# Kernel optimization log

Hardware: AMD Instinct MI355X
Metric: run time of the kernel (lower is better)

Reference implementation:

```python
import jax, jax.numpy as jnp
import numpy as np

T, H = 2048, 1024          # tokens, hidden_size
NH, NKV, D = 16, 4, 64     # heads, kv heads, head_dim
E, F = 8, 1024             # experts, intermediate_size
TOPK = 1
EPS = 1e-5
THETA = 500000.0
SCALE = D ** -0.5


def rmsnorm(x, w=None, eps=EPS):
    # fp32 accumulation like vLLM RMSNorm
    v = jnp.mean(x.astype(jnp.float32) ** 2, axis=-1, keepdims=True)
    y = x.astype(jnp.float32) * jax.lax.rsqrt(v + eps)
    y = y.astype(x.dtype)
    return y * w if w is not None else y


def setup_inputs() -> dict:
    key = jax.random.key(0)
    ks = jax.random.split(key, 12)
    s = 1.0 / np.sqrt(H)
    sf = 1.0 / np.sqrt(F)
    return {
        "positions": jnp.arange(T, dtype=jnp.int32),
        "hidden_states": jax.random.normal(ks[0], (T, H), jnp.float32),
        "ln1_w": jnp.ones((H,), jnp.float32),
        "ln2_w": jnp.ones((H,), jnp.float32),
        "wqkv": jax.random.normal(ks[1], (H, (NH + 2 * NKV) * D), jnp.float32) * s,
        "wo": jax.random.normal(ks[2], (NH * D, H), jnp.float32) * s,
        "router_w": jax.random.normal(ks[3], (H, E), jnp.float32) * s,
        "w_gate": jax.random.normal(ks[4], (E, H, F), jnp.float32) * s,
        "w_up": jax.random.normal(ks[5], (E, H, F), jnp.float32) * s,
        "w_down": jax.random.normal(ks[6], (E, F, H), jnp.float32) * sf,
        "sh_gate": jax.random.normal(ks[7], (H, F), jnp.float32) * s,
        "sh_up": jax.random.normal(ks[8], (H, F), jnp.float32) * s,
        "sh_down": jax.random.normal(ks[9], (F, H), jnp.float32) * sf,
    }


def reference(positions, hidden_states, ln1_w, ln2_w, wqkv, wo, router_w,
              w_gate, w_up, w_down, sh_gate, sh_up, sh_down):
    # --- input_layernorm (residual is None on first call) ---
    residual = hidden_states
    h = rmsnorm(hidden_states, ln1_w)

    # --- attention: qkv proj ---
    qkv = h @ wqkv
    q = qkv[:, : NH * D].reshape(T, NH, D)
    k = qkv[:, NH * D: (NH + NKV) * D].reshape(T, NKV, D)
    v = qkv[:, (NH + NKV) * D:].reshape(T, NKV, D)

    # --- neox-style RoPE ---
    half = D // 2
    inv_freq = 1.0 / (THETA ** (jnp.arange(half, dtype=jnp.float32) / half))
    ang = positions.astype(jnp.float32)[:, None] * inv_freq[None, :]
    cos = jnp.cos(ang)[:, None, :]  # [T,1,half]
    sin = jnp.sin(ang)[:, None, :]

    def rope(x):
        x1, x2 = x[..., :half], x[..., half:]
        return jnp.concatenate([x1 * cos - x2 * sin, x2 * cos + x1 * sin], axis=-1)

    q = rope(q)
    k = rope(k)

    # --- fp32 QK-RMSNorm (no weight), applied after RoPE as in source ---
    q = rmsnorm(q)
    k = rmsnorm(k)

    # --- GQA causal attention ---
    n_rep = NH // NKV
    kr = jnp.repeat(k, n_rep, axis=1)  # [T,NH,D]
    vr = jnp.repeat(v, n_rep, axis=1)
    scores = jnp.einsum('thd,shd->hts', q, kr) * SCALE  # [NH,T,T]
    causal = positions[:, None] >= positions[None, :]
    scores = jnp.where(causal[None], scores, -jnp.inf)
    attn = jax.nn.softmax(scores, axis=-1)
    ao = jnp.einsum('hts,shd->thd', attn, vr).reshape(T, NH * D)
    h = ao @ wo

    # --- post_attention_layernorm with fused residual add ---
    x = h + residual
    residual = x
    h = rmsnorm(x, ln2_w)

    # --- MoE: top-1 sigmoid router, router weight applied on input ---
    logits = h @ router_w                      # [T,E]
    score, idx = jax.lax.top_k(logits, TOPK)   # [T,1]
    gate = jax.nn.sigmoid(score.astype(jnp.float32)).astype(h.dtype)
    x_in = h * gate                            # apply_router_weight_on_input
    onehot = (idx == jnp.arange(E)[None, :]).astype(h.dtype)  # [T,E]
    g = jax.nn.silu(jnp.einsum('th,ehf->tef', x_in, w_gate)) \
        * jnp.einsum('th,ehf->tef', x_in, w_up)               # [T,E,F]
    out_e = jnp.einsum('tef,efh->teh', g, w_down)             # [T,E,H]
    routed = jnp.einsum('teh,te->th', out_e, onehot)

    # --- shared expert (SiLU MLP) ---
    shared = (jax.nn.silu(h @ sh_gate) * (h @ sh_up)) @ sh_down

    out = routed + shared
    return (out, residual)
```

## Files before the change

kernel.cpp:

```cpp
#include <hip/hip_runtime.h>
#include <hip/hip_bf16.h>
#include <cmath>
#include <cstdint>

#define T 2048
#define H 1024
#define NH 16
#define NKV 4
#define DH 64
#define NE 8
#define FF 1024
#define QKVN ((NH + 2 * NKV) * DH)
#define EPS 1e-5f
#define ATTN_SCALE 0.125f
#define LOG2E 1.44269504f
#define MBOUND 12.0f
#define ASPLIT 4

typedef short bf16x8 __attribute__((ext_vector_type(8)));
typedef float floatx4 __attribute__((ext_vector_type(4)));

__device__ __forceinline__ void gload16(const void* g, void* l) {
  __builtin_amdgcn_global_load_lds((const __attribute__((address_space(1))) void*)g,
                                   (__attribute__((address_space(3))) void*)l, 16, 0, 0);
}

__global__ __launch_bounds__(256) void rmsnorm1024(const float* __restrict__ x,
                                                   const float* __restrict__ w,
                                                   __hip_bfloat16* __restrict__ yb) {
  int row = blockIdx.x;
  const float4* x4 = (const float4*)(x + (size_t)row * H);
  float4 v = x4[threadIdx.x];
  float s = v.x * v.x + v.y * v.y + v.z * v.z + v.w * v.w;
  #pragma unroll
  for (int o = 32; o; o >>= 1) s += __shfl_down(s, o, 64);
  __shared__ float red[4];
  if ((threadIdx.x & 63) == 0) red[threadIdx.x >> 6] = s;
  __syncthreads();
  s = red[0] + red[1] + red[2] + red[3];
  float inv = rsqrtf(s * (1.0f / (float)H) + EPS);
  float4 wv = ((const float4*)w)[threadIdx.x];
  __hip_bfloat16* yp = yb + (size_t)row * H + threadIdx.x * 4;
  yp[0] = __float2bfloat16(v.x * inv * wv.x);
  yp[1] = __float2bfloat16(v.y * inv * wv.y);
  yp[2] = __float2bfloat16(v.z * inv * wv.z);
  yp[3] = __float2bfloat16(v.w * inv * wv.w);
}

__global__ __launch_bounds__(256) void rms_h2(const float* __restrict__ x,
                                              const float* __restrict__ w,
                                              float* __restrict__ yf,
                                              __hip_bfloat16* __restrict__ yb,
                                              int* __restrict__ counts_g) {
  int row = blockIdx.x;
  if (row == 0 && threadIdx.x < 2 * NE) counts_g[threadIdx.x] = 0;
  float4 v = ((const float4*)(x + (size_t)row * H))[threadIdx.x];
  float s = v.x * v.x + v.y * v.y + v.z * v.z + v.w * v.w;
  #pragma unroll
  for (int o = 32; o; o >>= 1) s += __shfl_down(s, o, 64);
  __shared__ float red[4];
  if ((threadIdx.x & 63) == 0) red[threadIdx.x >> 6] = s;
  __syncthreads();
  s = red[0] + red[1] + red[2] + red[3];
  float inv = rsqrtf(s * (1.0f / (float)H) + EPS);
  float4 wv = ((const float4*)w)[threadIdx.x];
  float o0 = v.x * inv * wv.x, o1 = v.y * inv * wv.y, o2 = v.z * inv * wv.z, o3 = v.w * inv * wv.w;
  ((float4*)(yf + (size_t)row * H))[threadIdx.x] = make_float4(o0, o1, o2, o3);
  __hip_bfloat16* yp = yb + (size_t)row * H + threadIdx.x * 4;
  yp[0] = __float2bfloat16(o0);
  yp[1] = __float2bfloat16(o1);
  yp[2] = __float2bfloat16(o2);
  yp[3] = __float2bfloat16(o3);
}

__global__ __launch_bounds__(256) void tcast9(const float* __restrict__ srcE,
                                              const float* __restrict__ srcS,
                                              __hip_bfloat16* __restrict__ dst, int R, int C,
                                              long long srcStride, long long dstStride,
                                              long long sBatch, long long dBatch) {
  int z = blockIdx.z;
  const float* src = (srcS && z == (int)gridDim.z - 1) ? srcS : srcE + (long long)z * sBatch;
  dst += (long long)z * dBatch;
  int c0 = blockIdx.x * 64, r0 = blockIdx.y * 32;
  __shared__ float tile[32][65];
  int tid = threadIdx.x;
  int lr = tid >> 4;
  int lc = (tid & 15) * 4;
  #pragma unroll
  for (int it = 0; it < 2; it++) {
    float4 v = *(const float4*)(src + (long long)(r0 + lr + it * 16) * srcStride + c0 + lc);
    tile[lr + it * 16][lc + 0] = v.x;
    tile[lr + it * 16][lc + 1] = v.y;
    tile[lr + it * 16][lc + 2] = v.z;
    tile[lr + it * 16][lc + 3] = v.w;
  }
  __syncthreads();
  int oc = tid >> 2;
  int rr = (tid & 3) * 8;
  short ov[8];
  #pragma unroll
  for (int i = 0; i < 8; i++) {
    __hip_bfloat16 b = __float2bfloat16(tile[rr + i][oc]);
    ov[i] = *(short*)&b;
  }
  *(bf16x8*)((short*)dst + (long long)(c0 + oc) * dstStride + r0 + rr) = *(bf16x8*)ov;
}

__global__ __launch_bounds__(256) void gemm_bf16(const __hip_bfloat16* __restrict__ A,
                                                 const __hip_bfloat16* __restrict__ A2,
                                                 const __hip_bfloat16* __restrict__ Bt,
                                                 void* __restrict__ Cout, void* __restrict__ Cout2,
                                                 int M, int N, int K, int out_bf16,
                                                 const int* __restrict__ row_offs,
                                                 long long strideB,
                                                 const int* __restrict__ permA,
                                                 const float* __restrict__ gatev,
                                                 const float* __restrict__ addC) {
  int e = blockIdx.z;
  bool sh = (A2 != nullptr && e == (int)gridDim.z - 1);
  int rbeg = 0, rend = M;
  const __hip_bfloat16* Ap = A;
  void* Cp = Cout;
  const int* pA = permA;
  if (sh) {
    Ap = A2; Cp = Cout2; pA = nullptr;
  } else if (row_offs) {
    rbeg = row_offs[e]; rend = row_offs[e + 1];
  }
  long long m0 = rbeg + (long long)blockIdx.y * 128;
  if (m0 >= rend) return;
  long long n0 = (long long)blockIdx.x * 64;
  const __hip_bfloat16* Bp = Bt + (long long)e * strideB;

  __shared__ unsigned short As[2][128 * 64];
  __shared__ unsigned short Bs[2][64 * 64];

  int tid = threadIdx.x;
  int lane = tid & 63, w = tid >> 6;
  int wr = (w >> 1) * 64, wc = (w & 1) * 32;
  int qd = lane >> 4, ln16 = lane & 15;
  int l7 = ln16 & 7;

  floatx4 acc[4][2];
  floatx4 zero = {0.f, 0.f, 0.f, 0.f};
  #pragma unroll
  for (int i = 0; i < 4; i++)
    #pragma unroll
    for (int j = 0; j < 2; j++) acc[i][j] = zero;

  int rowA[4], kcA[4];
  const unsigned short* Arow[4];
  const unsigned short* Brow[2];
  #pragma unroll
  for (int it = 0; it < 4; it++) {
    int chunk = tid + it * 256;
    rowA[it] = chunk >> 3;
    kcA[it] = ((chunk & 7) ^ (rowA[it] & 7)) * 8;
    long long ra = m0 + rowA[it];
    if (ra >= rend) ra = rend - 1;
    long long tok = pA ? (long long)pA[ra] : ra;
    Arow[it] = (const unsigned short*)Ap + tok * K;
  }
  #pragma unroll
  for (int it = 0; it < 2; it++)
    Brow[it] = (const unsigned short*)Bp + (n0 + rowA[it]) * K;

  #pragma unroll
  for (int it = 0; it < 4; it++)
    gload16(Arow[it] + kcA[it], As[0] + (tid + it * 256) * 8);
  #pragma unroll
  for (int it = 0; it < 2; it++)
    gload16(Brow[it] + kcA[it], Bs[0] + (tid + it * 256) * 8);
  __syncthreads();

  int cur = 0;
  for (int k0 = 0; k0 < K; k0 += 64) {
    int kn = k0 + 64;
    if (kn < K) {
      #pragma unroll
      for (int it = 0; it < 4; it++)
        gload16(Arow[it] + kn + kcA[it], As[cur ^ 1] + (tid + it * 256) * 8);
      #pragma unroll
      for (int it = 0; it < 2; it++)
        gload16(Brow[it] + kn + kcA[it], Bs[cur ^ 1] + (tid + it * 256) * 8);
    }
    const unsigned short* Ac = As[cur];
    const unsigned short* Bc = Bs[cur];
    #pragma unroll
    for (int s = 0; s < 2; s++) {
      bf16x8 af[4], bfr[2];
      #pragma unroll
      for (int i = 0; i < 4; i++) {
        int row = wr + i * 16 + ln16;
        af[i] = *(const bf16x8*)(Ac + row * 64 + (((s * 4 + qd) ^ l7) * 8));
      }
      #pragma unroll
      for (int j = 0; j < 2; j++) {
        int row = wc + j * 16 + ln16;
        bfr[j] = *(const bf16x8*)(Bc + row * 64 + (((s * 4 + qd) ^ l7) * 8));
      }
      #pragma unroll
      for (int i = 0; i < 4; i++)
        #pragma unroll
        for (int j = 0; j < 2; j++)
          acc[i][j] = __builtin_amdgcn_mfma_f32_16x16x32_bf16(af[i], bfr[j], acc[i][j], 0, 0, 0);
    }
    __syncthreads();
    cur ^= 1;
  }

  #pragma unroll
  for (int i = 0; i < 4; i++) {
    #pragma unroll
    for (int r = 0; r < 4; r++) {
      long long gm = m0 + wr + i * 16 + qd * 4 + r;
      if (gm < rend) {
        float gsc = 1.0f;
        if (pA && gatev) gsc = gatev[pA[gm]];
        #pragma unroll
        for (int j = 0; j < 2; j++) {
          long long gn = n0 + wc + j * 16 + ln16;
          float v = acc[i][j][r] * gsc;
          if (addC) v += addC[gm * N + gn];
          if (out_bf16)
            ((__hip_bfloat16*)Cp)[gm * N + gn] = __float2bfloat16(v);
          else
            ((float*)Cp)[gm * N + gn] = v;
        }
      }
    }
  }
}

__global__ __launch_bounds__(256) void gemm_qkv(const __hip_bfloat16* __restrict__ A,
                                                const __hip_bfloat16* __restrict__ Bt,
                                                const int* __restrict__ positions,
                                                __hip_bfloat16* __restrict__ Qb,
                                                __hip_bfloat16* __restrict__ Kb,
                                                __hip_bfloat16* __restrict__ VtG) {
  const int K = H;
  long long m0 = (long long)blockIdx.y * 128;
  long long n0 = (long long)blockIdx.x * 64;

  __shared__ unsigned short As[2][128 * 64];
  __shared__ unsigned short Bs[2][64 * 64];

  int tid = threadIdx.x;
  int lane = tid & 63, w = tid >> 6;
  int qd = lane >> 4, ln16 = lane & 15;
  int l7 = ln16 & 7;

  floatx4 acc[2][4];
  floatx4 zero = {0.f, 0.f, 0.f, 0.f};
  #pragma unroll
  for (int i = 0; i < 2; i++)
    #pragma unroll
    for (int j = 0; j < 4; j++) acc[i][j] = zero;

  int rowA[4], kcA[4];
  const unsigned short* Arow[4];
  const unsigned short* Brow[2];
  #pragma unroll
  for (int it = 0; it < 4; it++) {
    int chunk = tid + it * 256;
    rowA[it] = chunk >> 3;
    kcA[it] = ((chunk & 7) ^ (rowA[it] & 7)) * 8;
    Arow[it] = (const unsigned short*)A + (m0 + rowA[it]) * K;
  }
  #pragma unroll
  for (int it = 0; it < 2; it++)
    Brow[it] = (const unsigned short*)Bt + (n0 + rowA[it]) * K;

  #pragma unroll
  for (int it = 0; it < 4; it++)
    gload16(Arow[it] + kcA[it], As[0] + (tid + it * 256) * 8);
  #pragma unroll
  for (int it = 0; it < 2; it++)
    gload16(Brow[it] + kcA[it], Bs[0] + (tid + it * 256) * 8);
  __syncthreads();

  int cur = 0;
  for (int k0 = 0; k0 < K; k0 += 64) {
    int kn = k0 + 64;
    if (kn < K) {
      #pragma unroll
      for (int it = 0; it < 4; it++)
        gload16(Arow[it] + kn + kcA[it], As[cur ^ 1] + (tid + it * 256) * 8);
      #pragma unroll
      for (int it = 0; it < 2; it++)
        gload16(Brow[it] + kn + kcA[it], Bs[cur ^ 1] + (tid + it * 256) * 8);
    }
    const unsigned short* Ac = As[cur];
    const unsigned short* Bc = Bs[cur];
    #pragma unroll
    for (int s = 0; s < 2; s++) {
      bf16x8 af[2], bfr[4];
      #pragma unroll
      for (int i = 0; i < 2; i++) {
        int row = w * 32 + i * 16 + ln16;
        af[i] = *(const bf16x8*)(Ac + row * 64 + (((s * 4 + qd) ^ l7) * 8));
      }
      #pragma unroll
      for (int j = 0; j < 4; j++) {
        int row = j * 16 + ln16;
        bfr[j] = *(const bf16x8*)(Bc + row * 64 + (((s * 4 + qd) ^ l7) * 8));
      }
      #pragma unroll
      for (int i = 0; i < 2; i++)
        #pragma unroll
        for (int j = 0; j < 4; j++)
          acc[i][j] = __builtin_amdgcn_mfma_f32_16x16x32_bf16(af[i], bfr[j], acc[i][j], 0, 0, 0);
    }
    __syncthreads();
    cur ^= 1;
  }

  int hh = blockIdx.x;
  if (hh < NH + NKV) {
    bool isq = hh < NH;
    float invf0 = exp2f(-(float)ln16 * (18.93156857f / 32.0f));
    float invf1 = exp2f(-(float)(ln16 + 16) * (18.93156857f / 32.0f));
    #pragma unroll
    for (int i = 0; i < 2; i++) {
      #pragma unroll
      for (int r = 0; r < 4; r++) {
        int t = (int)m0 + w * 32 + i * 16 + qd * 4 + r;
        float pos = (float)positions[t];
        float c0, s0, c1, s1;
        __sincosf(pos * invf0, &s0, &c0);
        __sincosf(pos * invf1, &s1, &c1);
        float v0 = acc[i][0][r], v1 = acc[i][1][r], v2 = acc[i][2][r], v3 = acc[i][3][r];
        float ro0 = v0 * c0 - v2 * s0;
        float ro1 = v1 * c1 - v3 * s1;
        float ro2 = v2 * c0 + v0 * s0;
        float ro3 = v3 * c1 + v1 * s1;
        float sq = ro0 * ro0 + ro1 * ro1 + ro2 * ro2 + ro3 * ro3;
        sq += __shfl_xor(sq, 1, 64);
        sq += __shfl_xor(sq, 2, 64);
        sq += __shfl_xor(sq, 4, 64);
        sq += __shfl_xor(sq, 8, 64);
        float inv = rsqrtf(sq * (1.0f / (float)DH) + EPS);
        if (isq) inv *= (ATTN_SCALE * LOG2E);
        __hip_bfloat16* dst = isq ? (Qb + (size_t)t * (NH * DH) + hh * DH)
                                  : (Kb + (size_t)t * (NKV * DH) + (hh - NH) * DH);
        dst[0 * 16 + ln16] = __float2bfloat16(ro0 * inv);
        dst[1 * 16 + ln16] = __float2bfloat16(ro1 * inv);
        dst[2 * 16 + ln16] = __float2bfloat16(ro2 * inv);
        dst[3 * 16 + ln16] = __float2bfloat16(ro3 * inv);
      }
    }
  } else {
    unsigned short* sw = ((unsigned short*)As) + w * 2560;
    #pragma unroll
    for (int i = 0; i < 2; i++)
      #pragma unroll
      for (int j = 0; j < 4; j++)
        #pragma unroll
        for (int r = 0; r < 4; r++) {
          __hip_bfloat16 b = __float2bfloat16(acc[i][j][r]);
          sw[(j * 16 + ln16) * 40 + i * 16 + qd * 4 + r] = *(unsigned short*)&b;
        }
    int d = lane;
    int t0 = (int)m0 + w * 32;
    const unsigned short* sr = sw + d * 40;
    unsigned short* vd = (unsigned short*)VtG + (size_t)((hh - NH - NKV) * DH + d) * T + t0;
    #pragma unroll
    for (int kk = 0; kk < 4; kk++) {
      short tmp[8];
      #pragma unroll
      for (int q2 = 0; q2 < 8; q2++) tmp[q2] = sr[kk * 8 + q2];
      *(bf16x8*)(vd + kk * 8) = *(bf16x8*)tmp;
    }
  }
}

__global__ __launch_bounds__(256, 2) void attn_mfma(const __hip_bfloat16* __restrict__ Qb,
                                                    const __hip_bfloat16* __restrict__ Kbuf,
                                                    const __hip_bfloat16* __restrict__ VtG,
                                                    float* __restrict__ Opart,
                                                    float* __restrict__ Lpart) {
  int kvh = blockIdx.y;
  int qi = blockIdx.x;
  int sp = blockIdx.z;
  int q0 = qi * 64;
  int nt = qi + 1;
  if (sp >= nt) return;

  __shared__ unsigned short Ks[2][64 * 64];
  __shared__ unsigned short Vs[2][64 * 64];
  __shared__ unsigned short Ps[4 * 16 * 64];

  int tid = threadIdx.x;
  int lane = tid & 63, w = tid >> 6;
  int h = kvh * 4 + w;
  int qd = lane >> 4, ln16 = lane & 15;
  int l7 = ln16 & 7;
  unsigned short* Pw = Ps + w * 16 * 64;

  int r0 = tid >> 3;
  int sc = ((tid & 7) ^ (r0 & 7)) * 8;

  const unsigned short* KbP = (const unsigned short*)Kbuf;
  const unsigned short* VtP = (const unsigned short*)VtG;

  bf16x8 aq[4][2];
  #pragma unroll
  for (int rt = 0; rt < 4; rt++) {
    const unsigned short* qp =
        (const unsigned short*)Qb + (size_t)(q0 + rt * 16 + ln16) * (NH * DH) + h * DH;
    aq[rt][0] = *(const bf16x8*)(qp + qd * 8);
    aq[rt][1] = *(const bf16x8*)(qp + 32 + qd * 8);
  }

  bf16x8 ones;
  #pragma unroll
  for (int i = 0; i < 8; i++) ones[i] = (short)0x3F80;

  floatx4 O_[4][4], accl[4];
  floatx4 zero = {0.f, 0.f, 0.f, 0.f};
  #pragma unroll
  for (int rt = 0; rt < 4; rt++) {
    #pragma unroll
    for (int j = 0; j < 4; j++) O_[rt][j] = zero;
    accl[rt] = zero;
  }

  {
    int kb = sp * 64;
    gload16(KbP + (size_t)(kb + r0) * (NKV * DH) + kvh * DH + sc, Ks[0] + tid * 8);
    gload16(KbP + (size_t)(kb + r0 + 32) * (NKV * DH) + kvh * DH + sc, Ks[0] + tid * 8 + 2048);
    gload16(VtP + (size_t)(kvh * DH + r0) * T + kb + sc, Vs[0] + tid * 8);
    gload16(VtP + (size_t)(kvh * DH + r0 + 32) * T + kb + sc, Vs[0] + tid * 8 + 2048);
  }
  __syncthreads();

  int cur = 0;
  for (int kt = sp; kt < nt; kt += ASPLIT) {
    int ktn = kt + ASPLIT;
    if (ktn < nt) {
      int kb = ktn * 64;
      unsigned short* Kn = Ks[cur ^ 1];
      unsigned short* Vn = Vs[cur ^ 1];
      gload16(KbP + (size_t)(kb + r0) * (NKV * DH) + kvh * DH + sc, Kn + tid * 8);
      gload16(KbP + (size_t)(kb + r0 + 32) * (NKV * DH) + kvh * DH + sc, Kn + tid * 8 + 2048);
      gload16(VtP + (size_t)(kvh * DH + r0) * T + kb + sc, Vn + tid * 8);
      gload16(VtP + (size_t)(kvh * DH + r0 + 32) * T + kb + sc, Vn + tid * 8 + 2048);
    }
    const unsigned short* Kc = Ks[cur];
    const unsigned short* Vc = Vs[cur];
    int kb = kt * 64;

    #pragma unroll
    for (int rt = 0; rt < 4; rt++) {
      floatx4 S_[4];
      #pragma unroll
      for (int j = 0; j < 4; j++) S_[j] = zero;
      #pragma unroll
      for (int s = 0; s < 2; s++) {
        bf16x8 bk[4];
        #pragma unroll
        for (int j = 0; j < 4; j++)
          bk[j] = *(const bf16x8*)(Kc + (j * 16 + ln16) * 64 + (((s * 4 + qd) ^ l7) * 8));
        #pragma unroll
        for (int j = 0; j < 4; j++)
          S_[j] = __builtin_amdgcn_mfma_f32_16x16x32_bf16(aq[rt][s], bk[j], S_[j], 0, 0, 0);
      }

      int tq_base = q0 + rt * 16 + qd * 4;
      if (kb + 63 > q0 + rt * 16) {
        #pragma unroll
        for (int j = 0; j < 4; j++) {
          int tk = kb + j * 16 + ln16;
          #pragma unroll
          for (int r = 0; r < 4; r++)
            S_[j][r] = (tk <= tq_base + r) ? exp2f(S_[j][r] - MBOUND) : 0.f;
        }
      } else {
        #pragma unroll
        for (int j = 0; j < 4; j++)
          #pragma unroll
          for (int r = 0; r < 4; r++) S_[j][r] = exp2f(S_[j][r] - MBOUND);
      }

      #pragma unroll
      for (int j = 0; j < 4; j++)
        #pragma unroll
        for (int r = 0; r < 4; r++) {
          int row = qd * 4 + r;
          int pc = (((j * 2 + (ln16 >> 3)) ^ (row & 7)) * 8) + l7;
          __hip_bfloat16 pb = __float2bfloat16(S_[j][r]);
          Pw[row * 64 + pc] = *(unsigned short*)&pb;
        }

      #pragma unroll
      for (int s = 0; s < 2; s++) {
        bf16x8 ap = *(const bf16x8*)(Pw + ln16 * 64 + (((s * 4 + qd) ^ l7) * 8));
        bf16x8 bv[4];
        #pragma unroll
        for (int j = 0; j < 4; j++)
          bv[j] = *(const bf16x8*)(Vc + (j * 16 + ln16) * 64 + (((s * 4 + qd) ^ l7) * 8));
        #pragma unroll
        for (int j = 0; j < 4; j++)
          O_[rt][j] = __builtin_amdgcn_mfma_f32_16x16x32_bf16(ap, bv[j], O_[rt][j], 0, 0, 0);
        accl[rt] = __builtin_amdgcn_mfma_f32_16x16x32_bf16(ap, ones, accl[rt], 0, 0, 0);
      }
    }
    __syncthreads();
    cur ^= 1;
  }

  size_t pbase = ((size_t)(qi * NH + h) * ASPLIT + sp) * (64 * 64);
  #pragma unroll
  for (int rt = 0; rt < 4; rt++) {
    int rl_base = rt * 16 + qd * 4;
    #pragma unroll
    for (int j = 0; j < 4; j++)
      #pragma unroll
      for (int r = 0; r < 4; r++)
        Opart[pbase + (size_t)(rl_base + r) * 64 + j * 16 + ln16] = O_[rt][j][r];
  }
  if (ln16 == 0) {
    size_t lbase = ((size_t)(qi * NH + h) * ASPLIT + sp) * 64;
    #pragma unroll
    for (int rt = 0; rt < 4; rt++)
      #pragma unroll
      for (int r = 0; r < 4; r++) Lpart[lbase + rt * 16 + qd * 4 + r] = accl[rt][r];
  }
}

__global__ __launch_bounds__(256) void attn_combine(const float* __restrict__ Opart,
                                                    const float* __restrict__ Lpart,
                                                    __hip_bfloat16* __restrict__ ao) {
  int qi = blockIdx.x, h = blockIdx.y;
  int nv = (qi + 1 < ASPLIT) ? (qi + 1) : ASPLIT;
  int row = threadIdx.x >> 2;
  int c0 = (threadIdx.x & 3) * 16;
  size_t base = (size_t)(qi * NH + h) * ASPLIT * 4096;
  size_t lb = (size_t)(qi * NH + h) * ASPLIT * 64;
  float l = 0.f;
  float acc[16];
  #pragma unroll
  for (int i = 0; i < 16; i++) acc[i] = 0.f;
  for (int s = 0; s < nv; s++) {
    const float* Op = Opart + base + (size_t)s * 4096 + (size_t)row * 64 + c0;
    l += Lpart[lb + s * 64 + row];
    #pragma unroll
    for (int i = 0; i < 16; i += 4) {
      float4 v = *(const float4*)(Op + i);
      acc[i] += v.x; acc[i + 1] += v.y; acc[i + 2] += v.z; acc[i + 3] += v.w;
    }
  }
  float inv = 1.f / l;
  int t = qi * 64 + row;
  short ov[16];
  #pragma unroll
  for (int i = 0; i < 16; i++) {
    __hip_bfloat16 b = __float2bfloat16(acc[i] * inv);
    ov[i] = *(short*)&b;
  }
  short* dst = (short*)ao + (size_t)t * (NH * DH) + h * DH + c0;
  *(bf16x8*)dst = *(bf16x8*)&ov[0];
  *(bf16x8*)(dst + 8) = *(bf16x8*)&ov[8];
}

__global__ __launch_bounds__(256) void silumul_both(const __hip_bfloat16* __restrict__ gA2,
                                                    const __hip_bfloat16* __restrict__ gS2,
                                                    __hip_bfloat16* __restrict__ gP,
                                                    __hip_bfloat16* __restrict__ gPs,
                                                    int n8each) {
  int i = blockIdx.x * blockDim.x + threadIdx.x;
  const __hip_bfloat16* src = gA2;
  __hip_bfloat16* dst = gP;
  if (i >= n8each) {
    i -= n8each;
    src = gS2;
    dst = gPs;
  }
  int el = i * 8;
  int row = el >> 10;
  int c = el & (FF - 1);
  const unsigned short* g = (const unsigned short*)src + (size_t)row * (2 * FF) + c;
  bf16x8 a8 = *(const bf16x8*)g;
  bf16x8 b8 = *(const bf16x8*)(g + FF);
  short o8[8];
  #pragma unroll
  for (int k = 0; k < 8; k++) {
    short sa = a8[k], sb = b8[k];
    float av = __bfloat162float(*(__hip_bfloat16*)&sa);
    float bv = __bfloat162float(*(__hip_bfloat16*)&sb);
    __hip_bfloat16 ob = __float2bfloat16(av / (1.f + __expf(-av)) * bv);
    o8[k] = *(short*)&ob;
  }
  *(bf16x8*)((unsigned short*)dst + el) = *(bf16x8*)o8;
}

__global__ __launch_bounds__(64) void router_kernel(const float* __restrict__ h2,
                                                    const float* __restrict__ rw,
                                                    int* __restrict__ idx,
                                                    float* __restrict__ gate,
                                                    int* __restrict__ counts) {
  int t = blockIdx.x;
  int lane = threadIdx.x;
  float acc[NE] = {};
  for (int k = lane; k < H; k += 64) {
    float hv = h2[(long long)t * H + k];
    float4 r0 = *(const float4*)(rw + (long long)k * NE);
    float4 r1 = *(const float4*)(rw + (long long)k * NE + 4);
    acc[0] += hv * r0.x; acc[1] += hv * r0.y; acc[2] += hv * r0.z; acc[3] += hv * r0.w;
    acc[4] += hv * r1.x; acc[5] += hv * r1.y; acc[6] += hv * r1.z; acc[7] += hv * r1.w;
  }
  #pragma unroll
  for (int off = 32; off; off >>= 1)
    #pragma unroll
    for (int e2 = 0; e2 < NE; e2++) acc[e2] += __shfl_down(acc[e2], off, 64);
  if (lane == 0) {
    int best = 0;
    float bv = acc[0];
    #pragma unroll
    for (int e2 = 1; e2 < NE; e2++)
      if (acc[e2] > bv) { bv = acc[e2]; best = e2; }
    idx[t] = best;
    gate[t] = 1.f / (1.f + expf(-bv));
    atomicAdd(&counts[best], 1);
  }
}

__global__ __launch_bounds__(256) void assign_scan(const int* __restrict__ counts,
                                                   const int* __restrict__ idx,
                                                   int* __restrict__ offs,
                                                   int* __restrict__ cnt2,
                                                   int* __restrict__ perm,
                                                   int* __restrict__ pos) {
  __shared__ int offs_s[NE + 1];
  if (threadIdx.x == 0) {
    int s = 0;
    for (int e2 = 0; e2 < NE; e2++) { offs_s[e2] = s; offs[e2] = s; s += counts[e2]; }
    offs_s[NE] = s; offs[NE] = s;
  }
  __syncthreads();
  for (int t = threadIdx.x; t < T; t += 256) {
    int e2 = idx[t];
    int p = offs_s[e2] + atomicAdd(&cnt2[e2], 1);
    pos[t] = p;
    perm[p] = t;
  }
}

__global__ __launch_bounds__(256) void final_add_kernel(float* __restrict__ out,
                                                        const float* __restrict__ outp,
                                                        const int* __restrict__ pos) {
  int t = blockIdx.x;
  int p = pos[t];
  const float4* src = (const float4*)(outp + (long long)p * H);
  float4* dst = (float4*)(out + (long long)t * H);
  float4 a = dst[threadIdx.x];
  float4 b = src[threadIdx.x];
  a.x += b.x; a.y += b.y; a.z += b.z; a.w += b.w;
  dst[threadIdx.x] = a;
}

extern "C" void kernel_launch(void* const* d_in, const int* in_sizes, int n_in,
                              void* d_out, int out_size, void* d_ws, size_t ws_size,
                              hipStream_t stream) {
  const int* positions = (const int*)d_in[0];
  const float* hidden = (const float*)d_in[1];
  const float* ln1_w = (const float*)d_in[2];
  const float* ln2_w = (const float*)d_in[3];
  const float* wqkv = (const float*)d_in[4];
  const float* wo = (const float*)d_in[5];
  const float* router_w = (const float*)d_in[6];
  const float* w_gate = (const float*)d_in[7];
  const float* w_up = (const float*)d_in[8];
  const float* w_down = (const float*)d_in[9];
  const float* sh_gate = (const float*)d_in[10];
  const float* sh_up = (const float*)d_in[11];
  const float* sh_down = (const float*)d_in[12];

  float* out = (float*)d_out;
  float* resid = out + (size_t)T * H;

  char* p = (char*)d_ws;
  auto alloc = [&](size_t bytes) { char* r = p; p += (bytes + 255) & ~(size_t)255; return r; };

  float* qkv = (float*)alloc((size_t)T * QKVN * 4);
  float* h2 = (float*)alloc((size_t)T * H * 4);
  float* gb1 = (float*)alloc((size_t)T * H * 4);
  float* outp = (float*)alloc((size_t)T * H * 4);
  __hip_bfloat16* h1b = (__hip_bfloat16*)alloc((size_t)T * H * 2);
  __hip_bfloat16* aob = (__hip_bfloat16*)alloc((size_t)T * H * 2);
  __hip_bfloat16* h2b = (__hip_bfloat16*)alloc((size_t)T * H * 2);
  __hip_bfloat16* gA2 = (__hip_bfloat16*)alloc((size_t)T * 2 * FF * 2);
  __hip_bfloat16* gP = (__hip_bfloat16*)alloc((size_t)T * FF * 2);
  __hip_bfloat16* Qb = (__hip_bfloat16*)alloc((size_t)T * NH * DH * 2);
  __hip_bfloat16* Kb = (__hip_bfloat16*)alloc((size_t)T * NKV * DH * 2);
  __hip_bfloat16* VtG = (__hip_bfloat16*)alloc((size_t)NKV * DH * T * 2);
  __hip_bfloat16* wqkvT = (__hip_bfloat16*)alloc((size_t)H * QKVN * 2);
  __hip_bfloat16* woT = (__hip_bfloat16*)alloc((size_t)H * H * 2);
  __hip_bfloat16* wguT = (__hip_bfloat16*)alloc((size_t)9 * 2 * FF * H * 2);
  __hip_bfloat16* wdT = (__hip_bfloat16*)alloc((size_t)9 * H * FF * 2);
  int* counts = (int*)alloc(2 * NE * 4);
  int* cnt2 = counts + NE;
  int* offs = (int*)alloc((NE + 1) * 4);
  int* idx = (int*)alloc(T * 4);
  int* perm = (int*)alloc(T * 4);
  int* pos = (int*)alloc(T * 4);
  float* gate = (float*)alloc(T * 4);

  __hip_bfloat16* gS2 = (__hip_bfloat16*)gb1;
  __hip_bfloat16* gPs = h1b;

  float* Opart = qkv;
  float* Lpart = qkv + (size_t)(T / 64) * NH * ASPLIT * 4096;

  tcast9<<<dim3(QKVN / 64, H / 32, 1), 256, 0, stream>>>(wqkv, nullptr, wqkvT, H, QKVN, QKVN, H, 0, 0);
  tcast9<<<dim3(H / 64, H / 32, 1), 256, 0, stream>>>(wo, nullptr, woT, H, H, H, H, 0, 0);
  tcast9<<<dim3(FF / 64, H / 32, 9), 256, 0, stream>>>(w_gate, sh_gate, wguT, H, FF, FF, H,
                                                       (long long)H * FF, (long long)2 * H * FF);
  tcast9<<<dim3(FF / 64, H / 32, 9), 256, 0, stream>>>(w_up, sh_up, wguT + (size_t)FF * H, H, FF, FF, H,
                                                       (long long)H * FF, (long long)2 * H * FF);
  tcast9<<<dim3(H / 64, FF / 32, 9), 256, 0, stream>>>(w_down, sh_down, wdT, FF, H, H, FF,
                                                       (long long)FF * H, (long long)H * FF);

  rmsnorm1024<<<T, 256, 0, stream>>>(hidden, ln1_w, h1b);
  gemm_qkv<<<dim3(QKVN / 64, T / 128), 256, 0, stream>>>(h1b, wqkvT, positions, Qb, Kb, VtG);
  attn_mfma<<<dim3(T / 64, NKV, ASPLIT), 256, 0, stream>>>(Qb, Kb, VtG, Opart, Lpart);
  attn_combine<<<dim3(T / 64, NH), 256, 0, stream>>>(Opart, Lpart, aob);
  gemm_bf16<<<dim3(H / 64, T / 128, 1), 256, 0, stream>>>(aob, nullptr, woT, resid, nullptr,
                                                          T, H, H, 0, nullptr, 0, nullptr, nullptr,
                                                          hidden);
  rms_h2<<<T, 256, 0, stream>>>(resid, ln2_w, h2, h2b, counts);
  router_kernel<<<T, 64, 0, stream>>>(h2, router_w, idx, gate, counts);
  assign_scan<<<1, 256, 0, stream>>>(counts, idx, offs, cnt2, perm, pos);
  gemm_bf16<<<dim3(2 * FF / 64, T / 128, 9), 256, 0, stream>>>(h2b, h2b, wguT, gA2, gS2,
                                                               T, 2 * FF, H, 1, offs,
                                                               (long long)2 * H * FF, perm, gate,
                                                               nullptr);
  silumul_both<<<(2 * T * FF / 8) / 256, 256, 0, stream>>>(gA2, gS2, gP, gPs, T * FF / 8);
  gemm_bf16<<<dim3(H / 64, T / 128, 9), 256, 0, stream>>>(gP, gPs, wdT, outp, out,
                                                          T, H, FF, 0, offs, (long long)FF * H,
                                                          nullptr, nullptr, nullptr);
  final_add_kernel<<<T, 256, 0, stream>>>(out, outp, pos);
}
```

Measured before the change: 394.0 us.

## Fuse router into RMSNorm, scatter-add routed down-proj, merge weight casts

Computes the router logits, top-1 selection, sigmoid gate and expert counts inside the second RMSNorm kernel. This removes the fp32 h2 write and the separate router kernel. The counts reset moves into attn_combine, and the gate and up weight casts are merged into one 18-slice launch. The shared-expert down projection now runs first and writes `out`; the routed down projection then adds into `out` through perm, which removes the final_add kernel and the outp buffer. This serializes the shared and routed down GEMMs into two launches, and the non-atomic read-modify-write relies on each token having exactly one expert.

```diff
diff --git a/kernel.cpp b/kernel.cpp
--- a/kernel.cpp
+++ b/kernel.cpp
@@ -47,13 +47,14 @@
   yp[3] = __float2bfloat16(v.w * inv * wv.w);
 }
 
-__global__ __launch_bounds__(256) void rms_h2(const float* __restrict__ x,
-                                              const float* __restrict__ w,
-                                              float* __restrict__ yf,
-                                              __hip_bfloat16* __restrict__ yb,
-                                              int* __restrict__ counts_g) {
+__global__ __launch_bounds__(256) void rms_router(const float* __restrict__ x,
+                                                  const float* __restrict__ w,
+                                                  const float* __restrict__ rw,
+                                                  __hip_bfloat16* __restrict__ yb,
+                                                  int* __restrict__ idx,
+                                                  float* __restrict__ gate,
+                                                  int* __restrict__ counts) {
   int row = blockIdx.x;
-  if (row == 0 && threadIdx.x < 2 * NE) counts_g[threadIdx.x] = 0;
   float4 v = ((const float4*)(x + (size_t)row * H))[threadIdx.x];
   float s = v.x * v.x + v.y * v.y + v.z * v.z + v.w * v.w;
   #pragma unroll
@@ -65,22 +66,66 @@
   float inv = rsqrtf(s * (1.0f / (float)H) + EPS);
   float4 wv = ((const float4*)w)[threadIdx.x];
   float o0 = v.x * inv * wv.x, o1 = v.y * inv * wv.y, o2 = v.z * inv * wv.z, o3 = v.w * inv * wv.w;
-  ((float4*)(yf + (size_t)row * H))[threadIdx.x] = make_float4(o0, o1, o2, o3);
   __hip_bfloat16* yp = yb + (size_t)row * H + threadIdx.x * 4;
   yp[0] = __float2bfloat16(o0);
   yp[1] = __float2bfloat16(o1);
   yp[2] = __float2bfloat16(o2);
   yp[3] = __float2bfloat16(o3);
+  const float* r0 = rw + (size_t)threadIdx.x * 4 * NE;
+  float acc[NE];
+  float4 a0 = *(const float4*)(r0 + 0), a1 = *(const float4*)(r0 + 4);
+  float4 b0 = *(const float4*)(r0 + NE), b1 = *(const float4*)(r0 + NE + 4);
+  float4 c0 = *(const float4*)(r0 + 2 * NE), c1 = *(const float4*)(r0 + 2 * NE + 4);
+  float4 d0 = *(const float4*)(r0 + 3 * NE), d1 = *(const float4*)(r0 + 3 * NE + 4);
+  acc[0] = o0 * a0.x + o1 * b0.x + o2 * c0.x + o3 * d0.x;
+  acc[1] = o0 * a0.y + o1 * b0.y + o2 * c0.y + o3 * d0.y;
+  acc[2] = o0 * a0.z + o1 * b0.z + o2 * c0.z + o3 * d0.z;
+  acc[3] = o0 * a0.w + o1 * b0.w + o2 * c0.w + o3 * d0.w;
+  acc[4] = o0 * a1.x + o1 * b1.x + o2 * c1.x + o3 * d1.x;
+  acc[5] = o0 * a1.y + o1 * b1.y + o2 * c1.y + o3 * d1.y;
+  acc[6] = o0 * a1.z + o1 * b1.z + o2 * c1.z + o3 * d1.z;
+  acc[7] = o0 * a1.w + o1 * b1.w + o2 * c1.w + o3 * d1.w;
+  #pragma unroll
+  for (int off = 32; off; off >>= 1)
+    #pragma unroll
+    for (int e2 = 0; e2 < NE; e2++) acc[e2] += __shfl_down(acc[e2], off, 64);
+  __shared__ float redr[4][NE];
+  if ((threadIdx.x & 63) == 0)
+    #pragma unroll
+    for (int e2 = 0; e2 < NE; e2++) redr[threadIdx.x >> 6][e2] = acc[e2];
+  __syncthreads();
+  if (threadIdx.x == 0) {
+    int best = 0;
+    float bv = -3.4e38f;
+    #pragma unroll
+    for (int e2 = 0; e2 < NE; e2++) {
+      float l = redr[0][e2] + redr[1][e2] + redr[2][e2] + redr[3][e2];
+      if (l > bv) { bv = l; best = e2; }
+    }
+    idx[row] = best;
+    gate[row] = 1.f / (1.f + expf(-bv));
+    atomicAdd(&counts[best], 1);
+  }
 }
 
 __global__ __launch_bounds__(256) void tcast9(const float* __restrict__ srcE,
                                               const float* __restrict__ srcS,
+                                              const float* __restrict__ srcE2,
+                                              const float* __restrict__ srcS2,
                                               __hip_bfloat16* __restrict__ dst, int R, int C,
                                               long long srcStride, long long dstStride,
-                                              long long sBatch, long long dBatch) {
+                                              long long sBatch, long long dBatch,
+                                              long long d2Off, int nz1) {
   int z = blockIdx.z;
-  const float* src = (srcS && z == (int)gridDim.z - 1) ? srcS : srcE + (long long)z * sBatch;
-  dst += (long long)z * dBatch;
+  const float* src;
+  if (z < nz1) {
+    src = (srcS && z == nz1 - 1) ? srcS : srcE + (long long)z * sBatch;
+    dst += (long long)z * dBatch;
+  } else {
+    int z2 = z - nz1;
+    src = (srcS2 && z2 == nz1 - 1) ? srcS2 : srcE2 + (long long)z2 * sBatch;
+    dst += d2Off + (long long)z2 * dBatch;
+  }
   int c0 = blockIdx.x * 64, r0 = blockIdx.y * 32;
   __shared__ float tile[32][65];
   int tid = threadIdx.x;
@@ -115,7 +160,8 @@
                                                  long long strideB,
                                                  const int* __restrict__ permA,
                                                  const float* __restrict__ gatev,
-                                                 const float* __restrict__ addC) {
+                                                 const float* __restrict__ addC,
+                                                 const int* __restrict__ scatterPerm) {
   int e = blockIdx.z;
   bool sh = (A2 != nullptr && e == (int)gridDim.z - 1);
   int rbeg = 0, rend = M;
@@ -222,7 +268,10 @@
           long long gn = n0 + wc + j * 16 + ln16;
           float v = acc[i][j][r] * gsc;
           if (addC) v += addC[gm * N + gn];
-          if (out_bf16)
+          if (scatterPerm) {
+            float* op = (float*)Cp + (size_t)scatterPerm[gm] * N + gn;
+            *op += v;
+          } else if (out_bf16)
             ((__hip_bfloat16*)Cp)[gm * N + gn] = __float2bfloat16(v);
           else
             ((float*)Cp)[gm * N + gn] = v;
@@ -530,8 +579,10 @@
 
 __global__ __launch_bounds__(256) void attn_combine(const float* __restrict__ Opart,
                                                     const float* __restrict__ Lpart,
-                                                    __hip_bfloat16* __restrict__ ao) {
+                                                    __hip_bfloat16* __restrict__ ao,
+                                                    int* __restrict__ counts_g) {
   int qi = blockIdx.x, h = blockIdx.y;
+  if (qi == 0 && h == 0 && threadIdx.x < 2 * NE) counts_g[threadIdx.x] = 0;
   int nv = (qi + 1 < ASPLIT) ? (qi + 1) : ASPLIT;
   int row = threadIdx.x >> 2;
   int c0 = (threadIdx.x & 3) * 16;
@@ -594,37 +645,6 @@
   *(bf16x8*)((unsigned short*)dst + el) = *(bf16x8*)o8;
 }
 
-__global__ __launch_bounds__(64) void router_kernel(const float* __restrict__ h2,
-                                                    const float* __restrict__ rw,
-                                                    int* __restrict__ idx,
-                                                    float* __restrict__ gate,
-                                                    int* __restrict__ counts) {
-  int t = blockIdx.x;
-  int lane = threadIdx.x;
-  float acc[NE] = {};
-  for (int k = lane; k < H; k += 64) {
-    float hv = h2[(long long)t * H + k];
-    float4 r0 = *(const float4*)(rw + (long long)k * NE);
-    float4 r1 = *(const float4*)(rw + (long long)k * NE + 4);
-    acc[0] += hv * r0.x; acc[1] += hv * r0.y; acc[2] += hv * r0.z; acc[3] += hv * r0.w;
-    acc[4] += hv * r1.x; acc[5] += hv * r1.y; acc[6] += hv * r1.z; acc[7] += hv * r1.w;
-  }
-  #pragma unroll
-  for (int off = 32; off; off >>= 1)
-    #pragma unroll
-    for (int e2 = 0; e2 < NE; e2++) acc[e2] += __shfl_down(acc[e2], off, 64);
-  if (lane == 0) {
-    int best = 0;
-    float bv = acc[0];
-    #pragma unroll
-    for (int e2 = 1; e2 < NE; e2++)
-      if (acc[e2] > bv) { bv = acc[e2]; best = e2; }
-    idx[t] = best;
-    gate[t] = 1.f / (1.f + expf(-bv));
-    atomicAdd(&counts[best], 1);
-  }
-}
-
 __global__ __launch_bounds__(256) void assign_scan(const int* __restrict__ counts,
                                                    const int* __restrict__ idx,
                                                    int* __restrict__ offs,
@@ -644,19 +664,6 @@
     pos[t] = p;
     perm[p] = t;
   }
-}
-
-__global__ __launch_bounds__(256) void final_add_kernel(float* __restrict__ out,
-                                                        const float* __restrict__ outp,
-                                                        const int* __restrict__ pos) {
-  int t = blockIdx.x;
-  int p = pos[t];
-  const float4* src = (const float4*)(outp + (long long)p * H);
-  float4* dst = (float4*)(out + (long long)t * H);
-  float4 a = dst[threadIdx.x];
-  float4 b = src[threadIdx.x];
-  a.x += b.x; a.y += b.y; a.z += b.z; a.w += b.w;
-  dst[threadIdx.x] = a;
 }
 
 extern "C" void kernel_launch(void* const* d_in, const int* in_sizes, int n_in,
@@ -706,38 +713,43 @@
   int* pos = (int*)alloc(T * 4);
   float* gate = (float*)alloc(T * 4);
 
+  (void)h2; (void)outp; (void)pos;
+
   __hip_bfloat16* gS2 = (__hip_bfloat16*)gb1;
   __hip_bfloat16* gPs = h1b;
 
   float* Opart = qkv;
   float* Lpart = qkv + (size_t)(T / 64) * NH * ASPLIT * 4096;
 
-  tcast9<<<dim3(QKVN / 64, H / 32, 1), 256, 0, stream>>>(wqkv, nullptr, wqkvT, H, QKVN, QKVN, H, 0, 0);
-  tcast9<<<dim3(H / 64, H / 32, 1), 256, 0, stream>>>(wo, nullptr, woT, H, H, H, H, 0, 0);
-  tcast9<<<dim3(FF / 64, H / 32, 9), 256, 0, stream>>>(w_gate, sh_gate, wguT, H, FF, FF, H,
-                                                       (long long)H * FF, (long long)2 * H * FF);
-  tcast9<<<dim3(FF / 64, H / 32, 9), 256, 0, stream>>>(w_up, sh_up, wguT + (size_t)FF * H, H, FF, FF, H,
-                                                       (long long)H * FF, (long long)2 * H * FF);
-  tcast9<<<dim3(H / 64, FF / 32, 9), 256, 0, stream>>>(w_down, sh_down, wdT, FF, H, H, FF,
-                                                       (long long)FF * H, (long long)H * FF);
+  tcast9<<<dim3(QKVN / 64, H / 32, 1), 256, 0, stream>>>(wqkv, nullptr, nullptr, nullptr, wqkvT,
+                                                         H, QKVN, QKVN, H, 0, 0, 0, 1);
+  tcast9<<<dim3(H / 64, H / 32, 1), 256, 0, stream>>>(wo, nullptr, nullptr, nullptr, woT,
+                                                      H, H, H, H, 0, 0, 0, 1);
+  tcast9<<<dim3(FF / 64, H / 32, 18), 256, 0, stream>>>(w_gate, sh_gate, w_up, sh_up, wguT,
+                                                        H, FF, FF, H, (long long)H * FF,
+                                                        (long long)2 * H * FF, (long long)FF * H, 9);
+  tcast9<<<dim3(H / 64, FF / 32, 9), 256, 0, stream>>>(w_down, sh_down, nullptr, nullptr, wdT,
+                                                       FF, H, H, FF, (long long)FF * H,
+                                                       (long long)H * FF, 0, 9);
 
   rmsnorm1024<<<T, 256, 0, stream>>>(hidden, ln1_w, h1b);
   gemm_qkv<<<dim3(QKVN / 64, T / 128), 256, 0, stream>>>(h1b, wqkvT, positions, Qb, Kb, VtG);
   attn_mfma<<<dim3(T / 64, NKV, ASPLIT), 256, 0, stream>>>(Qb, Kb, VtG, Opart, Lpart);
-  attn_combine<<<dim3(T / 64, NH), 256, 0, stream>>>(Opart, Lpart, aob);
+  attn_combine<<<dim3(T / 64, NH), 256, 0, stream>>>(Opart, Lpart, aob, counts);
   gemm_bf16<<<dim3(H / 64, T / 128, 1), 256, 0, stream>>>(aob, nullptr, woT, resid, nullptr,
                                                           T, H, H, 0, nullptr, 0, nullptr, nullptr,
-                                                          hidden);
-  rms_h2<<<T, 256, 0, stream>>>(resid, ln2_w, h2, h2b, counts);
-  router_kernel<<<T, 64, 0, stream>>>(h2, router_w, idx, gate, counts);
+                                                          hidden, nullptr);
+  rms_router<<<T, 256, 0, stream>>>(resid, ln2_w, router_w, h2b, idx, gate, counts);
   assign_scan<<<1, 256, 0, stream>>>(counts, idx, offs, cnt2, perm, pos);
   gemm_bf16<<<dim3(2 * FF / 64, T / 128, 9), 256, 0, stream>>>(h2b, h2b, wguT, gA2, gS2,
                                                                T, 2 * FF, H, 1, offs,
                                                                (long long)2 * H * FF, perm, gate,
-                                                               nullptr);
+                                                               nullptr, nullptr);
   silumul_both<<<(2 * T * FF / 8) / 256, 256, 0, stream>>>(gA2, gS2, gP, gPs, T * FF / 8);
-  gemm_bf16<<<dim3(H / 64, T / 128, 9), 256, 0, stream>>>(gP, gPs, wdT, outp, out,
+  gemm_bf16<<<dim3(H / 64, T / 128, 1), 256, 0, stream>>>(gPs, nullptr, wdT + (size_t)8 * H * FF,
+                                                          out, nullptr, T, H, FF, 0, nullptr, 0,
+                                                          nullptr, nullptr, nullptr, nullptr);
+  gemm_bf16<<<dim3(H / 64, T / 128, 8), 256, 0, stream>>>(gP, nullptr, wdT, out, nullptr,
                                                           T, H, FF, 0, offs, (long long)FF * H,
-                                                          nullptr, nullptr, nullptr);
-  final_add_kernel<<<T, 256, 0, stream>>>(out, outp, pos);
-}
+                                                          nullptr, nullptr, nullptr, perm);
+}
```

Result: slower. 412.1 us (+4.6%).
